# Kernel optimization log

Measured on AMD Instinct MI355X. Metric: run time of the kernel, lower is better.

Reference implementation:

```python
import jax, jax.numpy as jnp
import numpy as np

L, DIM, S = 4, 17, 4
B, H, W = 4, 256, 256
BINSIZE = 16.0


def setup_inputs() -> dict:
    key = jax.random.key(0)
    k1, k2, k3, k4 = jax.random.split(key, 4)
    lut = jax.random.normal(k1, (L, DIM, DIM, DIM, DIM, S, S), dtype=jnp.float32)
    tri_index = jax.random.normal(k2, (24, 4), dtype=jnp.float32)
    weight = jax.random.uniform(k3, (B, L, H, W), dtype=jnp.float32)
    x = jax.random.uniform(k4, (B, 1, H, W), dtype=jnp.float32) * 255.0
    return {"lut": lut, "tri_index": tri_index, "weight": weight, "x": x, "scale_factor": S}


def _quadrilinear(lut, weight, x, s):
    # lut: [L, D, D, D, D, s, s]; weight: [B, L, H, W]; x: [B, 1, H, W] in [0,255]
    Bx, C, Hx, Wx = x.shape
    Lx, D = lut.shape[0], lut.shape[1]
    # reflection pad right/bottom by 1, take the 2x2 neighborhood -> 4 LUT coords
    xp = jnp.pad(x, ((0, 0), (0, 0), (0, 1), (0, 1)), mode="reflect")
    pix = jnp.stack([xp[:, :, :Hx, :Wx], xp[:, :, :Hx, 1:Wx + 1],
                     xp[:, :, 1:Hx + 1, :Wx], xp[:, :, 1:Hx + 1, 1:Wx + 1]], axis=-1)  # [B,C,H,W,4]
    t = pix / BINSIZE
    base_f = jnp.floor(t)
    frac = t - base_f                                   # [B,C,H,W,4] in [0,1)
    base = jnp.clip(base_f, 0, D - 2).astype(jnp.int32)  # [B,C,H,W,4]
    # 4D simplex (generalized tetrahedral) interpolation: sort fracs descending
    order = jnp.argsort(-frac, axis=-1)                 # [B,C,H,W,4]
    sf = jnp.take_along_axis(frac, order, axis=-1)      # sorted desc
    wts = jnp.stack([1.0 - sf[..., 0],
                     sf[..., 0] - sf[..., 1],
                     sf[..., 1] - sf[..., 2],
                     sf[..., 2] - sf[..., 3],
                     sf[..., 3]], axis=-1)              # [B,C,H,W,5]
    oneh = jax.nn.one_hot(order, 4, dtype=jnp.int32)    # [B,C,H,W,4,4]
    cum = jnp.cumsum(oneh, axis=-2)                     # vertex k offset = sum of top-k one-hots
    offs = jnp.concatenate([jnp.zeros_like(cum[..., :1, :]), cum], axis=-2)  # [B,C,H,W,5,4]
    vidx = base[..., None, :] + offs                    # [B,C,H,W,5,4]
    flat = ((vidx[..., 0] * D + vidx[..., 1]) * D + vidx[..., 2]) * D + vidx[..., 3]  # [B,C,H,W,5]
    lut_flat = lut.reshape(Lx, D ** 4, s * s)
    gathered = lut_flat[:, flat]                        # [L,B,C,H,W,5,s*s]
    interp = jnp.einsum("lbchwks,bchwk->lbchws", gathered, wts)  # [L,B,C,H,W,s*s]
    out = jnp.einsum("lbchws,blhw->bchws", interp, weight)       # [B,C,H,W,s*s]
    out = out.reshape(Bx, C, Hx, Wx, s, s).transpose(0, 1, 2, 4, 3, 5)
    return out.reshape(Bx, C, Hx * s, Wx * s)


def reference(lut, tri_index, weight, x, scale_factor):
    # tri_index encodes the precomputed simplex permutation table used by the CUDA
    # kernel; the reference derives the permutation analytically (argsort), so it is unused.
    return _quadrilinear(lut, weight, x, int(scale_factor))
```

## Files before the change

### kernel.cpp

```cpp
#include <hip/hip_runtime.h>
#include <hip/hip_fp16.h>

#define HH   256
#define WW   256
#define HWPX (HH * WW)
#define DD   17
#define D4   (17 * 17 * 17 * 17)
#define NL   4
#define SS   16
#define LUT_FLOATS  (NL * D4 * SS)
#define LUT_BYTES_H ((size_t)LUT_FLOATS * 2)

__global__ __launch_bounds__(256) void lut_transpose_h_kernel(
    const float4* __restrict__ src,
    ushort* __restrict__ dst)
{
    int t = blockIdx.x * blockDim.x + threadIdx.x;
    if (t >= D4 * NL * 4) return;
    int c4 = t & 3;
    int l  = (t >> 2) & 3;
    int v  = t >> 4;
    float4 r = src[(size_t)l * (D4 * 4) + (size_t)v * 4 + c4];
    ushort4 h;
    h.x = __half_as_ushort(__float2half_rn(r.x));
    h.y = __half_as_ushort(__float2half_rn(r.y));
    h.z = __half_as_ushort(__float2half_rn(r.z));
    h.w = __half_as_ushort(__float2half_rn(r.w));
    *((ushort4*)(dst + (size_t)t * 4)) = h;
}

__global__ __launch_bounds__(256) void lut4d_kernel_o(
    const ushort* __restrict__ lutT,
    const float* __restrict__ weight,
    const float* __restrict__ x,
    float* __restrict__ out)
{
    int tid = blockIdx.x * blockDim.x + threadIdx.x;
    int j = tid & 7;
    int p = tid >> 3;
    int b  = p >> 16;
    int hw = p & 65535;
    int h  = hw >> 8;
    int w  = hw & 255;

    const float* xb = x + b * HWPX;
    int h1 = (h + 1 < HH) ? (h + 1) : (HH - 2);
    int w1 = (w + 1 < WW) ? (w + 1) : (WW - 2);

    float pix0 = xb[h  * WW + w ];
    float pix1 = xb[h  * WW + w1];
    float pix2 = xb[h1 * WW + w ];
    float pix3 = xb[h1 * WW + w1];

    const float inv = 1.0f / 16.0f;
    float t0 = pix0 * inv, t1 = pix1 * inv, t2 = pix2 * inv, t3 = pix3 * inv;
    float bf0 = floorf(t0), bf1 = floorf(t1), bf2 = floorf(t2), bf3 = floorf(t3);
    float f0 = t0 - bf0, f1 = t1 - bf1, f2 = t2 - bf2, f3 = t3 - bf3;

    int b0 = min(max((int)bf0, 0), DD - 2);
    int b1 = min(max((int)bf1, 0), DD - 2);
    int b2 = min(max((int)bf2, 0), DD - 2);
    int b3 = min(max((int)bf3, 0), DD - 2);

    float s0f = f0, s1f = f1, s2f = f2, s3f = f3;
    int   s0s = 4913, s1s = 289, s2s = 17, s3s = 1;

#define CSWAP(fa, sa, fb, sb)                                          \
    do {                                                               \
        bool sw = (fb > fa) || ((fb == fa) && (sb > sa));              \
        float tf = fa; int ts = sa;                                    \
        if (sw) { fa = fb; sa = sb; fb = tf; sb = ts; }                \
    } while (0)

    CSWAP(s0f, s0s, s1f, s1s);
    CSWAP(s2f, s2s, s3f, s3s);
    CSWAP(s0f, s0s, s2f, s2s);
    CSWAP(s1f, s1s, s3f, s3s);
    CSWAP(s1f, s1s, s2f, s2s);
#undef CSWAP

    float wts[5];
    wts[0] = 1.0f - s0f;
    wts[1] = s0f - s1f;
    wts[2] = s1f - s2f;
    wts[3] = s2f - s3f;
    wts[4] = s3f;

    int flats[5];
    flats[0] = ((b0 * DD + b1) * DD + b2) * DD + b3;
    flats[1] = flats[0] + s0s;
    flats[2] = flats[1] + s1s;
    flats[3] = flats[2] + s2s;
    flats[4] = flats[3] + s3s;

    const float* wb = weight + b * (NL * HWPX) + hw;
    float wl[NL];
#pragma unroll
    for (int l = 0; l < NL; ++l) wl[l] = wb[l * HWPX];

    unsigned int r[5][NL];
#pragma unroll
    for (int k = 0; k < 5; ++k) {
        const ushort* vbase = lutT + (size_t)flats[k] * (NL * SS);
#pragma unroll
        for (int l = 0; l < NL; ++l) {
            r[k][l] = *((const unsigned int*)(vbase + l * SS + j * 2));
        }
    }

    float a0 = 0.f, a1 = 0.f;
#pragma unroll
    for (int k = 0; k < 5; ++k) {
#pragma unroll
        for (int l = 0; l < NL; ++l) {
            float c = wl[l] * wts[k];
            __half2 h01 = *reinterpret_cast<const __half2*>(&r[k][l]);
            float2 f01 = __half22float2(h01);
            a0 = fmaf(c, f01.x, a0);
            a1 = fmaf(c, f01.y, a1);
        }
    }

    float* ob = out + (size_t)b * (HH * 4) * (WW * 4)
                    + (size_t)(h * 4 + (j >> 1)) * (WW * 4)
                    + (w * 4) + ((j & 1) * 2);
    *((float2*)ob) = make_float2(a0, a1);
}

__global__ __launch_bounds__(256) void lut4d_kernel_fallback(
    const float* __restrict__ lut,
    const float* __restrict__ weight,
    const float* __restrict__ x,
    float* __restrict__ out)
{
    int p = blockIdx.x * blockDim.x + threadIdx.x;
    int b  = p >> 16;
    int hw = p & 65535;
    int h  = hw >> 8;
    int w  = hw & 255;

    const float* xb = x + b * HWPX;
    int h1 = (h + 1 < HH) ? (h + 1) : (HH - 2);
    int w1 = (w + 1 < WW) ? (w + 1) : (WW - 2);

    float pix0 = xb[h  * WW + w ];
    float pix1 = xb[h  * WW + w1];
    float pix2 = xb[h1 * WW + w ];
    float pix3 = xb[h1 * WW + w1];

    const float inv = 1.0f / 16.0f;
    float t0 = pix0 * inv, t1 = pix1 * inv, t2 = pix2 * inv, t3 = pix3 * inv;
    float bf0 = floorf(t0), bf1 = floorf(t1), bf2 = floorf(t2), bf3 = floorf(t3);
    float f0 = t0 - bf0, f1 = t1 - bf1, f2 = t2 - bf2, f3 = t3 - bf3;

    int b0 = min(max((int)bf0, 0), DD - 2);
    int b1 = min(max((int)bf1, 0), DD - 2);
    int b2 = min(max((int)bf2, 0), DD - 2);
    int b3 = min(max((int)bf3, 0), DD - 2);

    float s0f = f0, s1f = f1, s2f = f2, s3f = f3;
    int   s0s = 4913, s1s = 289, s2s = 17, s3s = 1;

#define CSWAP(fa, sa, fb, sb)                                          \
    do {                                                               \
        bool sw = (fb > fa) || ((fb == fa) && (sb > sa));              \
        float tf = fa; int ts = sa;                                    \
        if (sw) { fa = fb; sa = sb; fb = tf; sb = ts; }                \
    } while (0)

    CSWAP(s0f, s0s, s1f, s1s);
    CSWAP(s2f, s2s, s3f, s3s);
    CSWAP(s0f, s0s, s2f, s2s);
    CSWAP(s1f, s1s, s3f, s3s);
    CSWAP(s1f, s1s, s2f, s2s);
#undef CSWAP

    float wts[5] = { 1.0f - s0f, s0f - s1f, s1f - s2f, s2f - s3f, s3f };
    int flats[5];
    flats[0] = ((b0 * DD + b1) * DD + b2) * DD + b3;
    flats[1] = flats[0] + s0s;
    flats[2] = flats[1] + s1s;
    flats[3] = flats[2] + s2s;
    flats[4] = flats[3] + s3s;

    float acc[SS];
#pragma unroll
    for (int i = 0; i < SS; ++i) acc[i] = 0.0f;

    const float* wb = weight + b * (NL * HWPX) + hw;

#pragma unroll
    for (int l = 0; l < NL; ++l) {
        float wlv = wb[l * HWPX];
        const float* lbase = lut + (size_t)l * D4 * SS;
#pragma unroll
        for (int k = 0; k < 5; ++k) {
            float c = wlv * wts[k];
            const float4* row = (const float4*)(lbase + (size_t)flats[k] * SS);
#pragma unroll
            for (int q = 0; q < 4; ++q) {
                float4 rr = row[q];
                acc[q * 4 + 0] = fmaf(c, rr.x, acc[q * 4 + 0]);
                acc[q * 4 + 1] = fmaf(c, rr.y, acc[q * 4 + 1]);
                acc[q * 4 + 2] = fmaf(c, rr.z, acc[q * 4 + 2]);
                acc[q * 4 + 3] = fmaf(c, rr.w, acc[q * 4 + 3]);
            }
        }
    }

    float* ob = out + (size_t)b * (HH * 4) * (WW * 4) + (size_t)(h * 4) * (WW * 4) + (w * 4);
#pragma unroll
    for (int i = 0; i < 4; ++i) {
        *((float4*)(ob + (size_t)i * (WW * 4))) =
            make_float4(acc[i * 4 + 0], acc[i * 4 + 1], acc[i * 4 + 2], acc[i * 4 + 3]);
    }
}

extern "C" void kernel_launch(void* const* d_in, const int* in_sizes, int n_in,
                              void* d_out, int out_size, void* d_ws, size_t ws_size,
                              hipStream_t stream) {
    const float* lut    = (const float*)d_in[0];
    const float* weight = (const float*)d_in[2];
    const float* x      = (const float*)d_in[3];
    float* out          = (float*)d_out;

    dim3 block(256);

    if (ws_size >= LUT_BYTES_H) {
        ushort* lutT = (ushort*)d_ws;
        int n_chunks = D4 * NL * 4;
        dim3 grid_t((n_chunks + 255) / 256);
        hipLaunchKernelGGL(lut_transpose_h_kernel, grid_t, block, 0, stream,
                           (const float4*)lut, lutT);
        dim3 grid_main(8192);
        hipLaunchKernelGGL(lut4d_kernel_o, grid_main, block, 0, stream,
                           lutT, weight, x, out);
    } else {
        dim3 grid_main(1024);
        hipLaunchKernelGGL(lut4d_kernel_fallback, grid_main, block, 0, stream,
                           lut, weight, x, out);
    }
}
```

Before: 99.99 us.

## Split LUT levels across lanes with 16-byte loads and shuffle reduction

After: 99.80 us (median of 2 runs). About the same (-0.2%).

```diff
diff --git a/kernel.cpp b/kernel.cpp
--- a/kernel.cpp
+++ b/kernel.cpp
@@ -29,7 +29,7 @@
     *((ushort4*)(dst + (size_t)t * 4)) = h;
 }
 
-__global__ __launch_bounds__(256) void lut4d_kernel_o(
+__global__ __launch_bounds__(256) void lut4d_kernel_v(
     const ushort* __restrict__ lutT,
     const float* __restrict__ weight,
     const float* __restrict__ x,
@@ -42,6 +42,7 @@
     int hw = p & 65535;
     int h  = hw >> 8;
     int w  = hw & 255;
+    int l  = j >> 1;
 
     const float* xb = x + b * HWPX;
     int h1 = (h + 1 < HH) ? (h + 1) : (HH - 2);
@@ -51,6 +52,8 @@
     float pix1 = xb[h  * WW + w1];
     float pix2 = xb[h1 * WW + w ];
     float pix3 = xb[h1 * WW + w1];
+
+    float wlv = weight[(size_t)b * (NL * HWPX) + (size_t)l * HWPX + hw];
 
     const float inv = 1.0f / 16.0f;
     float t0 = pix0 * inv, t1 = pix1 * inv, t2 = pix2 * inv, t3 = pix3 * inv;
@@ -93,38 +96,58 @@
     flats[3] = flats[2] + s2s;
     flats[4] = flats[3] + s3s;
 
-    const float* wb = weight + b * (NL * HWPX) + hw;
-    float wl[NL];
-#pragma unroll
-    for (int l = 0; l < NL; ++l) wl[l] = wb[l * HWPX];
-
-    unsigned int r[5][NL];
+    uint4 r[5];
 #pragma unroll
     for (int k = 0; k < 5; ++k) {
         const ushort* vbase = lutT + (size_t)flats[k] * (NL * SS);
-#pragma unroll
-        for (int l = 0; l < NL; ++l) {
-            r[k][l] = *((const unsigned int*)(vbase + l * SS + j * 2));
-        }
-    }
-
-    float a0 = 0.f, a1 = 0.f;
+        r[k] = *((const uint4*)(vbase) + j);
+    }
+
+    float acc0 = 0.f, acc1 = 0.f, acc2 = 0.f, acc3 = 0.f;
+    float acc4 = 0.f, acc5 = 0.f, acc6 = 0.f, acc7 = 0.f;
 #pragma unroll
     for (int k = 0; k < 5; ++k) {
-#pragma unroll
-        for (int l = 0; l < NL; ++l) {
-            float c = wl[l] * wts[k];
-            __half2 h01 = *reinterpret_cast<const __half2*>(&r[k][l]);
-            float2 f01 = __half22float2(h01);
-            a0 = fmaf(c, f01.x, a0);
-            a1 = fmaf(c, f01.y, a1);
-        }
-    }
-
+        float c = wlv * wts[k];
+        float2 f0v = __half22float2(*reinterpret_cast<const __half2*>(&r[k].x));
+        float2 f1v = __half22float2(*reinterpret_cast<const __half2*>(&r[k].y));
+        float2 f2v = __half22float2(*reinterpret_cast<const __half2*>(&r[k].z));
+        float2 f3v = __half22float2(*reinterpret_cast<const __half2*>(&r[k].w));
+        acc0 = fmaf(c, f0v.x, acc0);
+        acc1 = fmaf(c, f0v.y, acc1);
+        acc2 = fmaf(c, f1v.x, acc2);
+        acc3 = fmaf(c, f1v.y, acc3);
+        acc4 = fmaf(c, f2v.x, acc4);
+        acc5 = fmaf(c, f2v.y, acc5);
+        acc6 = fmaf(c, f3v.x, acc6);
+        acc7 = fmaf(c, f3v.y, acc7);
+    }
+
+#define RED(mask)                                                      \
+    do {                                                               \
+        acc0 += __shfl_xor(acc0, mask, 64);                            \
+        acc1 += __shfl_xor(acc1, mask, 64);                            \
+        acc2 += __shfl_xor(acc2, mask, 64);                            \
+        acc3 += __shfl_xor(acc3, mask, 64);                            \
+        acc4 += __shfl_xor(acc4, mask, 64);                            \
+        acc5 += __shfl_xor(acc5, mask, 64);                            \
+        acc6 += __shfl_xor(acc6, mask, 64);                            \
+        acc7 += __shfl_xor(acc7, mask, 64);                            \
+    } while (0)
+    RED(2);
+    RED(4);
+#undef RED
+
+    int sel = j >> 1;
+    float o0 = (sel == 0) ? acc0 : (sel == 1) ? acc2 : (sel == 2) ? acc4 : acc6;
+    float o1 = (sel == 0) ? acc1 : (sel == 1) ? acc3 : (sel == 2) ? acc5 : acc7;
+
+    int c0  = (j & 1) * 8 + sel * 2;
+    int row = c0 >> 2;
+    int col = c0 & 3;
     float* ob = out + (size_t)b * (HH * 4) * (WW * 4)
-                    + (size_t)(h * 4 + (j >> 1)) * (WW * 4)
-                    + (w * 4) + ((j & 1) * 2);
-    *((float2*)ob) = make_float2(a0, a1);
+                    + (size_t)(h * 4 + row) * (WW * 4)
+                    + (w * 4) + col;
+    *((float2*)ob) = make_float2(o0, o1);
 }
 
 __global__ __launch_bounds__(256) void lut4d_kernel_fallback(
@@ -233,7 +256,7 @@
         hipLaunchKernelGGL(lut_transpose_h_kernel, grid_t, block, 0, stream,
                            (const float4*)lut, lutT);
         dim3 grid_main(8192);
-        hipLaunchKernelGGL(lut4d_kernel_o, grid_main, block, 0, stream,
+        hipLaunchKernelGGL(lut4d_kernel_v, grid_main, block, 0, stream,
                            lutT, weight, x, out);
     } else {
         dim3 grid_main(1024);
```
